# Kernel tuning notes

Hardware: AMD Instinct MI355X
Metric: run time of the kernel (lower is better)

Reference implementation:

```python
import jax, jax.numpy as jnp
import numpy as np

N_KERNELS = 11

def _kernel_mus(n):
    l = [1.0]
    if n == 1:
        return l
    b = 2.0 / (n - 1)
    l.append(1 - b / 2)
    for i in range(1, n - 1):
        l.append(l[i] - b)
    return l

def _kernel_sigmas(n):
    b = 2.0 / (n - 1)
    l = [0.0001]
    if n == 1:
        return l
    l += [0.5 * b] * (n - 1)
    return l

MU = jnp.asarray(np.array(_kernel_mus(N_KERNELS), dtype=np.float32))      # [K]
SIGMA = jnp.asarray(np.array(_kernel_sigmas(N_KERNELS), dtype=np.float32))  # [K]


def setup_inputs() -> dict:
    key = jax.random.key(0)
    k1, k2, k3, k4 = jax.random.split(key, 4)
    B, Q, D, V, E = 256, 32, 512, 100000, 300
    return {
        "query_tokens": jax.random.randint(k1, (B, Q), 0, V),
        "doc_tokens": jax.random.randint(k2, (B, D), 0, V),
        "emb": jax.random.normal(k3, (V, E), dtype=jnp.float32),
        "fc_w": jax.random.normal(k4, (1, N_KERNELS), dtype=jnp.float32),
        "fc_b": jnp.zeros((1,), dtype=jnp.float32),
    }


def reference(query_tokens, doc_tokens, emb, fc_w, fc_b):
    q_mask = (query_tokens > 0).astype(jnp.float32)  # [B,Q]
    d_mask = (doc_tokens > 0).astype(jnp.float32)    # [B,D]

    qe = emb[query_tokens]  # [B,Q,E]
    de = emb[doc_tokens]    # [B,D,E]

    # Cosine match matrix (CosineMatrixAttention: L2-normalize with tiny eps)
    qn = qe / (jnp.linalg.norm(qe, axis=-1, keepdims=True) + 1e-13)
    dn = de / (jnp.linalg.norm(de, axis=-1, keepdims=True) + 1e-13)
    mm = jnp.einsum("bqe,bde->bqd", qn, dn)  # [B,Q,D]

    mask = q_mask[:, :, None] * d_mask[:, None, :]  # [B,Q,D]
    mm = mm * mask

    # Gaussian RBF kernel pooling: [B,Q,D,K]
    diff = mm[..., None] - MU[None, None, None, :]
    rbf = jnp.exp(-jnp.square(diff) / (2.0 * jnp.square(SIGMA)[None, None, None, :]))
    rbf = rbf * mask[..., None]

    query_kernels = rbf.sum(axis=2)  # [B,Q,K]
    log_qk = jnp.log(jnp.maximum(query_kernels, 1e-10)) * 0.01
    # NOTE: original code computes a masked version but (bug) sums the UNMASKED
    # log_query_kernels; we faithfully replicate that.
    kernels = log_qk.sum(axis=1)  # [B,K]

    score = kernels @ fc_w.T + fc_b  # [B,1]
    return score
```

## Files before the change

kernel.cpp:

```cpp
#include <hip/hip_runtime.h>
#include <hip/hip_bf16.h>
#include <math.h>


#define NB 256
#define NQ 32
#define ND 512
#define NE 300
#define NF4 75
#define LROW 328
#define CHUNK 64
#define NCHUNK 8
#define NT 512

typedef __bf16 bf16x8 __attribute__((ext_vector_type(8)));
typedef __bf16 bf16x4 __attribute__((ext_vector_type(4)));
typedef float f32x4 __attribute__((ext_vector_type(4)));

__global__ __launch_bounds__(NT, 1) void knrm_kernel(
    const int* __restrict__ qtok,
    const int* __restrict__ dtok,
    const float* __restrict__ emb,
    const float* __restrict__ fcw,
    const float* __restrict__ fcb,
    float* __restrict__ out)
{
  __shared__ __align__(16) __bf16 qlds[NQ][LROW];
  __shared__ __align__(16) __bf16 dlds[CHUNK][LROW];
  __shared__ float qscale[NQ];
  __shared__ float dscale[CHUNK];
  __shared__ float qk[NQ][11];
  __shared__ float red;

  const int b = blockIdx.x;
  const int t = threadIdx.x;
  const int lane = t & 63;
  const int w = t >> 6;

  if (t < NQ * 11 && (t % 11) != 0) (&qk[0][0])[t] = 0.0f;
  if (t == 0) red = 0.0f;

  {
    const int r = t >> 4;
    const int j = t & 15;
    const int tq = qtok[b * NQ + r];
    const float4* rowp = (const float4*)(emb + (size_t)tq * NE);
    float ss = 0.0f;
    for (int c = j; c < NF4; c += 16) {
      float4 v = rowp[c];
      ss += v.x * v.x + v.y * v.y + v.z * v.z + v.w * v.w;
      bf16x4 h;
      h[0] = (__bf16)v.x; h[1] = (__bf16)v.y; h[2] = (__bf16)v.z; h[3] = (__bf16)v.w;
      *(bf16x4*)&qlds[r][4 * c] = h;
    }
    if (j < 5) {
      bf16x4 z = {(__bf16)0.0f, (__bf16)0.0f, (__bf16)0.0f, (__bf16)0.0f};
      *(bf16x4*)&qlds[r][NE + 4 * j] = z;
    }
    ss += __shfl_xor(ss, 1, 16);
    ss += __shfl_xor(ss, 2, 16);
    ss += __shfl_xor(ss, 4, 16);
    ss += __shfl_xor(ss, 8, 16);
    if (j == 0) qscale[r] = (tq > 0) ? 1.0f / (sqrtf(ss) + 1e-13f) : 0.0f;

    int cnt = 0;
    for (int jj = 0; jj < 32; ++jj) {
      int td = dtok[b * ND + j + 16 * jj];
      cnt += (tq > 0 && td == tq) ? 1 : 0;
    }
    cnt += __shfl_xor(cnt, 1, 16);
    cnt += __shfl_xor(cnt, 2, 16);
    cnt += __shfl_xor(cnt, 4, 16);
    cnt += __shfl_xor(cnt, 8, 16);
    if (j == 0) qk[r][0] = (float)cnt;
  }

  const int mt = w >> 2;
  const int nt = w & 3;
  const int l15 = lane & 15;
  const int l4 = lane >> 4;

  float rbfacc[4][10];
  #pragma unroll
  for (int r4 = 0; r4 < 4; ++r4)
    #pragma unroll
    for (int k = 0; k < 10; ++k) rbfacc[r4][k] = 0.0f;

  const __bf16* aptr = &qlds[mt * 16 + l15][l4 * 8];
  const __bf16* bptr = &dlds[nt * 16 + l15][l4 * 8];

  const float muk[10] = {0.9f, 0.7f, 0.5f, 0.3f, 0.1f,
                         -0.1f, -0.3f, -0.5f, -0.7f, -0.9f};

  for (int ch = 0; ch < NCHUNK; ++ch) {
    __syncthreads();
    {
      const int r = t >> 3;
      const int j = t & 7;
      const int td = dtok[b * ND + ch * CHUNK + r];
      const float4* rowp = (const float4*)(emb + (size_t)td * NE);
      float ss = 0.0f;
      for (int c = j; c < NF4; c += 8) {
        float4 v = rowp[c];
        ss += v.x * v.x + v.y * v.y + v.z * v.z + v.w * v.w;
        bf16x4 h;
        h[0] = (__bf16)v.x; h[1] = (__bf16)v.y; h[2] = (__bf16)v.z; h[3] = (__bf16)v.w;
        *(bf16x4*)&dlds[r][4 * c] = h;
      }
      if (j < 5) {
        bf16x4 z = {(__bf16)0.0f, (__bf16)0.0f, (__bf16)0.0f, (__bf16)0.0f};
        *(bf16x4*)&dlds[r][NE + 4 * j] = z;
      }
      ss += __shfl_xor(ss, 1, 8);
      ss += __shfl_xor(ss, 2, 8);
      ss += __shfl_xor(ss, 4, 8);
      if (j == 0) dscale[r] = (td > 0) ? 1.0f / (sqrtf(ss) + 1e-13f) : 0.0f;
    }
    __syncthreads();

    f32x4 acc = {0.0f, 0.0f, 0.0f, 0.0f};
    #pragma unroll
    for (int k = 0; k < 10; ++k) {
      bf16x8 av = *(const bf16x8*)(aptr + k * 32);
      bf16x8 bv = *(const bf16x8*)(bptr + k * 32);
      acc = __builtin_amdgcn_mfma_f32_16x16x32_bf16(av, bv, acc, 0, 0, 0);
    }

    const float ds = dscale[nt * 16 + l15];
    #pragma unroll
    for (int r4 = 0; r4 < 4; ++r4) {
      const float qs = qscale[mt * 16 + l4 * 4 + r4];
      const float s = qs * ds;
      const float mm = (s == 0.0f) ? 1e8f : acc[r4] * s;
      #pragma unroll
      for (int k = 0; k < 10; ++k) {
        float d = mm - muk[k];
        rbfacc[r4][k] += __builtin_amdgcn_exp2f(d * d * -72.13475204444817f);
      }
    }
  }

  #pragma unroll
  for (int r4 = 0; r4 < 4; ++r4) {
    #pragma unroll
    for (int k = 0; k < 10; ++k) {
      float v = rbfacc[r4][k];
      v += __shfl_xor(v, 1, 16);
      v += __shfl_xor(v, 2, 16);
      v += __shfl_xor(v, 4, 16);
      v += __shfl_xor(v, 8, 16);
      if (l15 == 0) atomicAdd(&qk[mt * 16 + l4 * 4 + r4][k + 1], v);
    }
  }
  __syncthreads();

  float v = 0.0f;
  if (t < NQ * 11) {
    int q = t / 11;
    int k = t % 11;
    v = logf(fmaxf(qk[q][k], 1e-10f)) * 0.01f * fcw[k];
  }
  #pragma unroll
  for (int off = 1; off < 64; off <<= 1) v += __shfl_xor(v, off, 64);
  if (lane == 0) atomicAdd(&red, v);
  __syncthreads();
  if (t == 0) out[b] = red + fcb[0];
}

extern "C" void kernel_launch(void* const* d_in, const int* in_sizes, int n_in,
                              void* d_out, int out_size, void* d_ws, size_t ws_size,
                              hipStream_t stream) {
  const int* qtok = (const int*)d_in[0];
  const int* dtok = (const int*)d_in[1];
  const float* emb = (const float*)d_in[2];
  const float* fcw = (const float*)d_in[3];
  const float* fcb = (const float*)d_in[4];
  float* out = (float*)d_out;
  knrm_kernel<<<NB, NT, 0, stream>>>(qtok, dtok, emb, fcw, fcb, out);
}
```

Baseline: 226.1 us.

## Split documents across four blocks per batch and load doc fragments into registers

Each batch is now handled by four blocks, each covering 128 documents, and a small second kernel combines the partial kernel sums through workspace memory and applies the log and linear layer. Document embeddings are loaded straight into MFMA B-fragments in registers rather than staged through LDS chunks, which removes the per-chunk barriers. Each wave reuses its doc fragments across both query tiles. The aim is more blocks for occupancy on a GPU with many CUs and less LDS and sync traffic, at the cost of an extra launch, a global partial-sum round trip, and the query embeddings being reloaded by all four split blocks.

```diff
diff --git a/kernel.cpp b/kernel.cpp
--- a/kernel.cpp
+++ b/kernel.cpp
@@ -7,164 +7,172 @@
 #define NQ 32
 #define ND 512
 #define NE 300
-#define NF4 75
 #define LROW 328
-#define CHUNK 64
-#define NCHUNK 8
-#define NT 512
+#define SPLITS 4
+#define DPB 128
+#define NT 256
+#define NK 11
+#define QK_SZ (NQ * NK)
 
 typedef __bf16 bf16x8 __attribute__((ext_vector_type(8)));
 typedef __bf16 bf16x4 __attribute__((ext_vector_type(4)));
 typedef float f32x4 __attribute__((ext_vector_type(4)));
 
-__global__ __launch_bounds__(NT, 1) void knrm_kernel(
+__global__ __launch_bounds__(NT, 3) void knrm_main(
     const int* __restrict__ qtok,
     const int* __restrict__ dtok,
     const float* __restrict__ emb,
-    const float* __restrict__ fcw,
-    const float* __restrict__ fcb,
-    float* __restrict__ out)
+    float* __restrict__ partial)
 {
   __shared__ __align__(16) __bf16 qlds[NQ][LROW];
-  __shared__ __align__(16) __bf16 dlds[CHUNK][LROW];
   __shared__ float qscale[NQ];
-  __shared__ float dscale[CHUNK];
-  __shared__ float qk[NQ][11];
-  __shared__ float red;
+  __shared__ float qkl[QK_SZ];
 
-  const int b = blockIdx.x;
-  const int t = threadIdx.x;
+  const int b    = blockIdx.x >> 2;
+  const int sp   = blockIdx.x & 3;
+  const int t    = threadIdx.x;
   const int lane = t & 63;
-  const int w = t >> 6;
+  const int w    = t >> 6;
+  const int quad = lane >> 4;
+  const int l15  = lane & 15;
 
-  if (t < NQ * 11 && (t % 11) != 0) (&qk[0][0])[t] = 0.0f;
-  if (t == 0) red = 0.0f;
+  for (int i = t; i < QK_SZ; i += NT)
+    if (i % NK) qkl[i] = 0.0f;
 
   {
-    const int r = t >> 4;
-    const int j = t & 15;
+    const int r = t >> 3;
+    const int j = t & 7;
     const int tq = qtok[b * NQ + r];
     const float4* rowp = (const float4*)(emb + (size_t)tq * NE);
     float ss = 0.0f;
-    for (int c = j; c < NF4; c += 16) {
+    for (int c = j; c < 75; c += 8) {
       float4 v = rowp[c];
       ss += v.x * v.x + v.y * v.y + v.z * v.z + v.w * v.w;
       bf16x4 h;
       h[0] = (__bf16)v.x; h[1] = (__bf16)v.y; h[2] = (__bf16)v.z; h[3] = (__bf16)v.w;
       *(bf16x4*)&qlds[r][4 * c] = h;
     }
-    if (j < 5) {
-      bf16x4 z = {(__bf16)0.0f, (__bf16)0.0f, (__bf16)0.0f, (__bf16)0.0f};
-      *(bf16x4*)&qlds[r][NE + 4 * j] = z;
-    }
-    ss += __shfl_xor(ss, 1, 16);
-    ss += __shfl_xor(ss, 2, 16);
-    ss += __shfl_xor(ss, 4, 16);
-    ss += __shfl_xor(ss, 8, 16);
+    if (j < 5) { bf16x4 z = {}; *(bf16x4*)&qlds[r][NE + 4 * j] = z; }
+    ss += __shfl_xor(ss, 1, 8);
+    ss += __shfl_xor(ss, 2, 8);
+    ss += __shfl_xor(ss, 4, 8);
     if (j == 0) qscale[r] = (tq > 0) ? 1.0f / (sqrtf(ss) + 1e-13f) : 0.0f;
 
     int cnt = 0;
-    for (int jj = 0; jj < 32; ++jj) {
-      int td = dtok[b * ND + j + 16 * jj];
+    #pragma unroll 4
+    for (int i = 0; i < 16; ++i) {
+      int td = dtok[b * ND + sp * DPB + j + 8 * i];
       cnt += (tq > 0 && td == tq) ? 1 : 0;
     }
-    cnt += __shfl_xor(cnt, 1, 16);
-    cnt += __shfl_xor(cnt, 2, 16);
-    cnt += __shfl_xor(cnt, 4, 16);
-    cnt += __shfl_xor(cnt, 8, 16);
-    if (j == 0) qk[r][0] = (float)cnt;
+    cnt += __shfl_xor(cnt, 1, 8);
+    cnt += __shfl_xor(cnt, 2, 8);
+    cnt += __shfl_xor(cnt, 4, 8);
+    if (j == 0) qkl[r * NK] = (float)cnt;
   }
-
-  const int mt = w >> 2;
-  const int nt = w & 3;
-  const int l15 = lane & 15;
-  const int l4 = lane >> 4;
-
-  float rbfacc[4][10];
-  #pragma unroll
-  for (int r4 = 0; r4 < 4; ++r4)
-    #pragma unroll
-    for (int k = 0; k < 10; ++k) rbfacc[r4][k] = 0.0f;
-
-  const __bf16* aptr = &qlds[mt * 16 + l15][l4 * 8];
-  const __bf16* bptr = &dlds[nt * 16 + l15][l4 * 8];
+  __syncthreads();
 
   const float muk[10] = {0.9f, 0.7f, 0.5f, 0.3f, 0.1f,
                          -0.1f, -0.3f, -0.5f, -0.7f, -0.9f};
 
-  for (int ch = 0; ch < NCHUNK; ++ch) {
-    __syncthreads();
+  float rbf[2][4][10] = {};
+
+  #pragma unroll 1
+  for (int gi = 0; gi < 2; ++gi) {
+    const int g = w + 4 * gi;
+    const int d = sp * DPB + g * 16 + l15;
+    const int td = dtok[b * ND + d];
+    const float* rowf = emb + (size_t)td * NE;
+
+    float ss = 0.0f;
+    bf16x8 bfrag[10];
+    #pragma unroll
+    for (int kk = 0; kk < 9; ++kk) {
+      const float4* p = (const float4*)(rowf + kk * 32 + quad * 8);
+      float4 v0 = p[0];
+      float4 v1 = p[1];
+      ss += v0.x * v0.x + v0.y * v0.y + v0.z * v0.z + v0.w * v0.w;
+      ss += v1.x * v1.x + v1.y * v1.y + v1.z * v1.z + v1.w * v1.w;
+      bf16x8 h;
+      h[0] = (__bf16)v0.x; h[1] = (__bf16)v0.y; h[2] = (__bf16)v0.z; h[3] = (__bf16)v0.w;
+      h[4] = (__bf16)v1.x; h[5] = (__bf16)v1.y; h[6] = (__bf16)v1.z; h[7] = (__bf16)v1.w;
+      bfrag[kk] = h;
+    }
     {
-      const int r = t >> 3;
-      const int j = t & 7;
-      const int td = dtok[b * ND + ch * CHUNK + r];
-      const float4* rowp = (const float4*)(emb + (size_t)td * NE);
-      float ss = 0.0f;
-      for (int c = j; c < NF4; c += 8) {
-        float4 v = rowp[c];
-        ss += v.x * v.x + v.y * v.y + v.z * v.z + v.w * v.w;
-        bf16x4 h;
-        h[0] = (__bf16)v.x; h[1] = (__bf16)v.y; h[2] = (__bf16)v.z; h[3] = (__bf16)v.w;
-        *(bf16x4*)&dlds[r][4 * c] = h;
+      const int base = 288 + quad * 8;
+      bf16x8 h;
+      #pragma unroll
+      for (int j = 0; j < 8; ++j) {
+        const int e = base + j;
+        float v = (e < NE) ? rowf[e] : 0.0f;
+        ss += v * v;
+        h[j] = (__bf16)v;
       }
-      if (j < 5) {
-        bf16x4 z = {(__bf16)0.0f, (__bf16)0.0f, (__bf16)0.0f, (__bf16)0.0f};
-        *(bf16x4*)&dlds[r][NE + 4 * j] = z;
+      bfrag[9] = h;
+    }
+    ss += __shfl_xor(ss, 16);
+    ss += __shfl_xor(ss, 32);
+    const float dsc = (td > 0) ? 1.0f / (sqrtf(ss) + 1e-13f) : 0.0f;
+
+    #pragma unroll
+    for (int mt = 0; mt < 2; ++mt) {
+      f32x4 acc = {};
+      #pragma unroll
+      for (int kk = 0; kk < 10; ++kk) {
+        bf16x8 av = *(const bf16x8*)&qlds[mt * 16 + l15][kk * 32 + quad * 8];
+        acc = __builtin_amdgcn_mfma_f32_16x16x32_bf16(av, bfrag[kk], acc, 0, 0, 0);
       }
-      ss += __shfl_xor(ss, 1, 8);
-      ss += __shfl_xor(ss, 2, 8);
-      ss += __shfl_xor(ss, 4, 8);
-      if (j == 0) dscale[r] = (td > 0) ? 1.0f / (sqrtf(ss) + 1e-13f) : 0.0f;
-    }
-    __syncthreads();
-
-    f32x4 acc = {0.0f, 0.0f, 0.0f, 0.0f};
-    #pragma unroll
-    for (int k = 0; k < 10; ++k) {
-      bf16x8 av = *(const bf16x8*)(aptr + k * 32);
-      bf16x8 bv = *(const bf16x8*)(bptr + k * 32);
-      acc = __builtin_amdgcn_mfma_f32_16x16x32_bf16(av, bv, acc, 0, 0, 0);
-    }
-
-    const float ds = dscale[nt * 16 + l15];
-    #pragma unroll
-    for (int r4 = 0; r4 < 4; ++r4) {
-      const float qs = qscale[mt * 16 + l4 * 4 + r4];
-      const float s = qs * ds;
-      const float mm = (s == 0.0f) ? 1e8f : acc[r4] * s;
       #pragma unroll
-      for (int k = 0; k < 10; ++k) {
-        float d = mm - muk[k];
-        rbfacc[r4][k] += __builtin_amdgcn_exp2f(d * d * -72.13475204444817f);
+      for (int r = 0; r < 4; ++r) {
+        const float qs = qscale[mt * 16 + quad * 4 + r];
+        const float s = qs * dsc;
+        const float mm = (s == 0.0f) ? 1e8f : acc[r] * s;
+        #pragma unroll
+        for (int k = 0; k < 10; ++k) {
+          float dd = mm - muk[k];
+          rbf[mt][r][k] += __builtin_amdgcn_exp2f(dd * dd * -72.13475204444817f);
+        }
       }
     }
   }
 
   #pragma unroll
-  for (int r4 = 0; r4 < 4; ++r4) {
+  for (int mt = 0; mt < 2; ++mt)
     #pragma unroll
-    for (int k = 0; k < 10; ++k) {
-      float v = rbfacc[r4][k];
-      v += __shfl_xor(v, 1, 16);
-      v += __shfl_xor(v, 2, 16);
-      v += __shfl_xor(v, 4, 16);
-      v += __shfl_xor(v, 8, 16);
-      if (l15 == 0) atomicAdd(&qk[mt * 16 + l4 * 4 + r4][k + 1], v);
-    }
-  }
+    for (int r = 0; r < 4; ++r)
+      #pragma unroll
+      for (int k = 0; k < 10; ++k) {
+        float v = rbf[mt][r][k];
+        v += __shfl_xor(v, 1);
+        v += __shfl_xor(v, 2);
+        v += __shfl_xor(v, 4);
+        v += __shfl_xor(v, 8);
+        if (l15 == 0)
+          atomicAdd(&qkl[(mt * 16 + quad * 4 + r) * NK + k + 1], v);
+      }
   __syncthreads();
 
-  float v = 0.0f;
-  if (t < NQ * 11) {
-    int q = t / 11;
-    int k = t % 11;
-    v = logf(fmaxf(qk[q][k], 1e-10f)) * 0.01f * fcw[k];
+  float* pp = partial + ((size_t)b * SPLITS + sp) * QK_SZ;
+  for (int i = t; i < QK_SZ; i += NT) pp[i] = qkl[i];
+}
+
+__global__ __launch_bounds__(64) void knrm_epi(
+    const float* __restrict__ partial,
+    const float* __restrict__ fcw,
+    const float* __restrict__ fcb,
+    float* __restrict__ out)
+{
+  const int b = blockIdx.x;
+  const int lane = threadIdx.x;
+  const float* pb = partial + (size_t)b * SPLITS * QK_SZ;
+  float acc = 0.0f;
+  for (int i = lane; i < QK_SZ; i += 64) {
+    float s = pb[i] + pb[i + QK_SZ] + pb[i + 2 * QK_SZ] + pb[i + 3 * QK_SZ];
+    int k = i % NK;
+    acc += logf(fmaxf(s, 1e-10f)) * 0.01f * fcw[k];
   }
   #pragma unroll
-  for (int off = 1; off < 64; off <<= 1) v += __shfl_xor(v, off, 64);
-  if (lane == 0) atomicAdd(&red, v);
-  __syncthreads();
-  if (t == 0) out[b] = red + fcb[0];
+  for (int off = 1; off < 64; off <<= 1) acc += __shfl_xor(acc, off);
+  if (lane == 0) out[b] = acc + fcb[0];
 }
 
 extern "C" void kernel_launch(void* const* d_in, const int* in_sizes, int n_in,
@@ -176,5 +184,8 @@
   const float* fcw = (const float*)d_in[3];
   const float* fcb = (const float*)d_in[4];
   float* out = (float*)d_out;
-  knrm_kernel<<<NB, NT, 0, stream>>>(qtok, dtok, emb, fcw, fcb, out);
+  float* partial = (float*)d_ws;
+
+  knrm_main<<<NB * SPLITS, NT, 0, stream>>>(qtok, dtok, emb, partial);
+  knrm_epi<<<NB, 64, 0, stream>>>(partial, fcw, fcb, out);
 }
```

Result: slower. 301.1 us (+33.2%).

## Split document dimension across two blocks per batch with epilogue reduction kernel

Applied to the files above, without the earlier changes.

Each batch item's 512 document tokens are now split across two workgroups, so 512 workgroups run instead of 256 on a GPU with many compute units. Each workgroup writes its partial query-kernel sums to workspace, and a second small kernel adds the halves, applies the log, and takes the dot with the fc weights. This raises parallelism and shortens each block's serial chunk loop. The cost is loading and normalizing the query embeddings twice, an extra kernel launch, and a global round-trip for the partial sums.

```diff
diff --git a/kernel.cpp b/kernel.cpp
--- a/kernel.cpp
+++ b/kernel.cpp
@@ -9,36 +9,37 @@
 #define NE 300
 #define NF4 75
 #define LROW 328
+#define SPLITS 2
+#define DPB 256
 #define CHUNK 64
-#define NCHUNK 8
+#define NCHUNK 4
 #define NT 512
+#define NK 11
+#define QK_SZ (NQ * NK)
 
 typedef __bf16 bf16x8 __attribute__((ext_vector_type(8)));
 typedef __bf16 bf16x4 __attribute__((ext_vector_type(4)));
 typedef float f32x4 __attribute__((ext_vector_type(4)));
 
-__global__ __launch_bounds__(NT, 1) void knrm_kernel(
+__global__ __launch_bounds__(NT, 1) void knrm_main(
     const int* __restrict__ qtok,
     const int* __restrict__ dtok,
     const float* __restrict__ emb,
-    const float* __restrict__ fcw,
-    const float* __restrict__ fcb,
-    float* __restrict__ out)
+    float* __restrict__ partial)
 {
   __shared__ __align__(16) __bf16 qlds[NQ][LROW];
   __shared__ __align__(16) __bf16 dlds[CHUNK][LROW];
   __shared__ float qscale[NQ];
   __shared__ float dscale[CHUNK];
-  __shared__ float qk[NQ][11];
-  __shared__ float red;
+  __shared__ float qkl[QK_SZ];
 
-  const int b = blockIdx.x;
-  const int t = threadIdx.x;
+  const int b    = blockIdx.x >> 1;
+  const int sp   = blockIdx.x & 1;
+  const int t    = threadIdx.x;
   const int lane = t & 63;
-  const int w = t >> 6;
+  const int w    = t >> 6;
 
-  if (t < NQ * 11 && (t % 11) != 0) (&qk[0][0])[t] = 0.0f;
-  if (t == 0) red = 0.0f;
+  if (t < QK_SZ && (t % NK) != 0) qkl[t] = 0.0f;
 
   {
     const int r = t >> 4;
@@ -54,7 +55,7 @@
       *(bf16x4*)&qlds[r][4 * c] = h;
     }
     if (j < 5) {
-      bf16x4 z = {(__bf16)0.0f, (__bf16)0.0f, (__bf16)0.0f, (__bf16)0.0f};
+      bf16x4 z = {};
       *(bf16x4*)&qlds[r][NE + 4 * j] = z;
     }
     ss += __shfl_xor(ss, 1, 16);
@@ -64,21 +65,22 @@
     if (j == 0) qscale[r] = (tq > 0) ? 1.0f / (sqrtf(ss) + 1e-13f) : 0.0f;
 
     int cnt = 0;
-    for (int jj = 0; jj < 32; ++jj) {
-      int td = dtok[b * ND + j + 16 * jj];
+    #pragma unroll
+    for (int jj = 0; jj < DPB / 16; ++jj) {
+      int td = dtok[b * ND + sp * DPB + j + 16 * jj];
       cnt += (tq > 0 && td == tq) ? 1 : 0;
     }
     cnt += __shfl_xor(cnt, 1, 16);
     cnt += __shfl_xor(cnt, 2, 16);
     cnt += __shfl_xor(cnt, 4, 16);
     cnt += __shfl_xor(cnt, 8, 16);
-    if (j == 0) qk[r][0] = (float)cnt;
+    if (j == 0) qkl[r * NK] = (float)cnt;
   }
 
-  const int mt = w >> 2;
-  const int nt = w & 3;
+  const int mt  = w >> 2;
+  const int nt  = w & 3;
   const int l15 = lane & 15;
-  const int l4 = lane >> 4;
+  const int l4  = lane >> 4;
 
   float rbfacc[4][10];
   #pragma unroll
@@ -92,12 +94,13 @@
   const float muk[10] = {0.9f, 0.7f, 0.5f, 0.3f, 0.1f,
                          -0.1f, -0.3f, -0.5f, -0.7f, -0.9f};
 
+  #pragma unroll 1
   for (int ch = 0; ch < NCHUNK; ++ch) {
     __syncthreads();
     {
       const int r = t >> 3;
       const int j = t & 7;
-      const int td = dtok[b * ND + ch * CHUNK + r];
+      const int td = dtok[b * ND + sp * DPB + ch * CHUNK + r];
       const float4* rowp = (const float4*)(emb + (size_t)td * NE);
       float ss = 0.0f;
       for (int c = j; c < NF4; c += 8) {
@@ -108,7 +111,7 @@
         *(bf16x4*)&dlds[r][4 * c] = h;
       }
       if (j < 5) {
-        bf16x4 z = {(__bf16)0.0f, (__bf16)0.0f, (__bf16)0.0f, (__bf16)0.0f};
+        bf16x4 z = {};
         *(bf16x4*)&dlds[r][NE + 4 * j] = z;
       }
       ss += __shfl_xor(ss, 1, 8);
@@ -118,7 +121,7 @@
     }
     __syncthreads();
 
-    f32x4 acc = {0.0f, 0.0f, 0.0f, 0.0f};
+    f32x4 acc = {};
     #pragma unroll
     for (int k = 0; k < 10; ++k) {
       bf16x8 av = *(const bf16x8*)(aptr + k * 32);
@@ -141,30 +144,40 @@
   }
 
   #pragma unroll
-  for (int r4 = 0; r4 < 4; ++r4) {
+  for (int r4 = 0; r4 < 4; ++r4)
     #pragma unroll
     for (int k = 0; k < 10; ++k) {
       float v = rbfacc[r4][k];
-      v += __shfl_xor(v, 1, 16);
-      v += __shfl_xor(v, 2, 16);
-      v += __shfl_xor(v, 4, 16);
-      v += __shfl_xor(v, 8, 16);
-      if (l15 == 0) atomicAdd(&qk[mt * 16 + l4 * 4 + r4][k + 1], v);
+      v += __shfl_xor(v, 1);
+      v += __shfl_xor(v, 2);
+      v += __shfl_xor(v, 4);
+      v += __shfl_xor(v, 8);
+      if (l15 == 0) atomicAdd(&qkl[(mt * 16 + l4 * 4 + r4) * NK + k + 1], v);
     }
-  }
   __syncthreads();
 
-  float v = 0.0f;
-  if (t < NQ * 11) {
-    int q = t / 11;
-    int k = t % 11;
-    v = logf(fmaxf(qk[q][k], 1e-10f)) * 0.01f * fcw[k];
+  float* pp = partial + ((size_t)b * SPLITS + sp) * QK_SZ;
+  for (int i = t; i < QK_SZ; i += NT) pp[i] = qkl[i];
+}
+
+__global__ __launch_bounds__(64) void knrm_epi(
+    const float* __restrict__ partial,
+    const float* __restrict__ fcw,
+    const float* __restrict__ fcb,
+    float* __restrict__ out)
+{
+  const int b = blockIdx.x;
+  const int lane = threadIdx.x;
+  const float* pb = partial + (size_t)b * SPLITS * QK_SZ;
+  float acc = 0.0f;
+  for (int i = lane; i < QK_SZ; i += 64) {
+    float s = pb[i] + pb[i + QK_SZ];
+    int k = i % NK;
+    acc += logf(fmaxf(s, 1e-10f)) * 0.01f * fcw[k];
   }
   #pragma unroll
-  for (int off = 1; off < 64; off <<= 1) v += __shfl_xor(v, off, 64);
-  if (lane == 0) atomicAdd(&red, v);
-  __syncthreads();
-  if (t == 0) out[b] = red + fcb[0];
+  for (int off = 1; off < 64; off <<= 1) acc += __shfl_xor(acc, off);
+  if (lane == 0) out[b] = acc + fcb[0];
 }
 
 extern "C" void kernel_launch(void* const* d_in, const int* in_sizes, int n_in,
@@ -176,5 +189,8 @@
   const float* fcw = (const float*)d_in[3];
   const float* fcb = (const float*)d_in[4];
   float* out = (float*)d_out;
-  knrm_kernel<<<NB, NT, 0, stream>>>(qtok, dtok, emb, fcw, fcb, out);
+  float* partial = (float*)d_ws;
+
+  knrm_main<<<NB * SPLITS, NT, 0, stream>>>(qtok, dtok, emb, partial);
+  knrm_epi<<<NB, 64, 0, stream>>>(partial, fcw, fcb, out);
 }
```

New measurement: 206.9 us. 1.09x faster.
